# Kernel optimization log

Measured on AMD Instinct MI355X. Metric: run time of the kernel, lower is better.

## Reference

```python
import jax, jax.numpy as jnp
import numpy as np

N_NODES = 32768
N_EDGES = 196608
N_GRAPHS = 256
DEG = 6
HID = 128
RVD = 16
EMB = HID - RVD   # atom/bond embedding dim = hidden - random_vec_dim
VOCAB = 128
TGT = 256
DEPTH = 5
N_AGG = 4         # mean, max, min, std
N_SC = 3          # identity, amplification, attenuation
EPS = 1e-5


def setup_inputs() -> dict:
    key = jax.random.key(0)
    ks = jax.random.split(key, 12)

    def g(i, shape, scale=0.05):
        return jax.random.normal(ks[i], shape, dtype=jnp.float32) * scale

    return {
        "atom_feats": jax.random.randint(ks[0], (N_NODES, 9), 0, 100),
        "bond_feats": jax.random.randint(ks[1], (N_EDGES, 3), 0, 4),
        "src": jax.random.randint(ks[2], (N_EDGES,), 0, N_NODES),
        # every node receives exactly DEG messages (DGL reduce requires in-edges)
        "dst": jnp.repeat(jnp.arange(N_NODES), DEG),
        "graph_ids": jnp.repeat(jnp.arange(N_GRAPHS), N_NODES // N_GRAPHS),
        "n_graphs": N_GRAPHS,
        "rand_x": jax.random.normal(ks[3], (N_NODES, RVD), dtype=jnp.float32),   # std=1.0
        "rand_edge": jax.random.normal(ks[4], (N_EDGES, RVD), dtype=jnp.float32),
        "atom_emb": g(5, (9, VOCAB, EMB)),
        "bond_emb": g(6, (3, VOCAB, EMB)),
        "pre_W": g(7, (DEPTH, 3 * HID, HID)),
        "pre_b": jnp.zeros((DEPTH, HID), jnp.float32),
        "post_W": g(8, (DEPTH, (N_AGG * N_SC + 1) * HID, HID)),
        "post_b": jnp.zeros((DEPTH, HID), jnp.float32),
        "ro_W1": g(9, (3 * HID, HID)),
        "ro_b1": jnp.zeros((HID,), jnp.float32),
        "ro_W2": g(10, (HID, TGT)),
        "ro_b2": jnp.zeros((TGT,), jnp.float32),
    }


def reference(atom_feats, bond_feats, src, dst, graph_ids, n_graphs,
              rand_x, rand_edge, atom_emb, bond_emb,
              pre_W, pre_b, post_W, post_b, ro_W1, ro_b1, ro_W2, ro_b2):
    n = atom_feats.shape[0]
    # OGB-style encoders: sum of per-column embeddings, then concat random vec
    h = jnp.concatenate([atom_emb[jnp.arange(9), atom_feats].sum(1), rand_x], -1)   # [N, HID]
    ef = jnp.concatenate([bond_emb[jnp.arange(3), bond_feats].sum(1), rand_edge], -1)  # [E, HID]

    deg = jax.ops.segment_sum(jnp.ones((dst.shape[0],), h.dtype), dst, n)
    degc = jnp.maximum(deg, 1.0)[:, None]
    logD = jnp.log(deg + 1.0)[:, None]                 # avg_d['log'] = 1.0
    inv_logD = jnp.where(logD > 0, 1.0 / jnp.maximum(logD, EPS), 0.0)

    def layer(hc, p):
        pW, pb, qW, qb = p
        # pretrans MLP on [src_feat, dst_feat, edge_feat]; last_activation = activation (relu)
        z = jnp.concatenate([hc[src], hc[dst], ef], -1)          # [E, 3*HID]
        e = jax.nn.relu(z @ pW + pb)                             # [E, HID]
        s = jax.ops.segment_sum(e, dst, n)
        mean = s / degc
        mean_sq = jax.ops.segment_sum(e * e, dst, n) / degc
        mx = jax.ops.segment_max(e, dst, n)
        mn = jax.ops.segment_min(e, dst, n)
        std = jnp.sqrt(jax.nn.relu(mean_sq - mean * mean) + EPS)
        agg = jnp.concatenate([mean, mx, mn, std], -1)           # [N, 4*HID]
        scaled = jnp.concatenate([agg, agg * logD, agg * inv_logD], -1)  # [N, 12*HID]
        h_new = jnp.concatenate([hc, scaled], -1) @ qW + qb + hc  # posttrans (linear) + residual
        return h_new, None

    h, _ = jax.lax.scan(layer, h, (pre_W, pre_b, post_W, post_b))

    # multi-aggregator readout: mean, sum, max per graph
    cnt = jnp.maximum(jax.ops.segment_sum(jnp.ones((n,), h.dtype), graph_ids, n_graphs), 1.0)[:, None]
    gsum = jax.ops.segment_sum(h, graph_ids, n_graphs)
    gmax = jax.ops.segment_max(h, graph_ids, n_graphs)
    r = jnp.concatenate([gsum / cnt, gsum, gmax], -1)            # [G, 3*HID]
    return jax.nn.relu(r @ ro_W1 + ro_b1) @ ro_W2 + ro_b2        # [G, TGT]
```

## Files before the change

### kernel.cpp

```cpp
#include <hip/hip_runtime.h>
#include <hip/hip_bf16.h>

#define N_NODES 32768
#define N_EDGES 196608
#define N_GRAPHS 256
#define DEG 6
#define HID 128
#define RVD 16
#define EMB 112
#define VOCAB 128
#define TGT 256
#define DEPTH 5

#define LOG7 1.9459101090932196f
#define ILOG7 0.5138983423697507f

typedef __hip_bfloat16 bf16;
using frag_ab = __attribute__((ext_vector_type(8))) short;
using frag_cd = __attribute__((ext_vector_type(4))) float;
typedef float f32x2 __attribute__((ext_vector_type(2)));

static __device__ __forceinline__ float b2f(bf16 x) { return __bfloat162float(x); }
static __device__ __forceinline__ bf16  f2b(float x) { return __float2bfloat16(x); }
static __device__ __forceinline__ float us2f(unsigned short u) {
    unsigned int x = ((unsigned int)u) << 16;
    return __uint_as_float(x);
}
static __device__ __forceinline__ unsigned short f2us(float x) {
    bf16 b = __float2bfloat16(x);
    return *reinterpret_cast<unsigned short*>(&b);
}

#define PB_ENC  16384
#define PB_WB   (PB_ENC + 640)
#define PB_WC   (PB_WB + 1600)
#define PB_WR   (PB_WC + 80)
#define PB_CODE (PB_WR + 768)
#define PB_T    (PB_CODE + 320)

__global__ __launch_bounds__(256) void prep_k(const int* __restrict__ af, const float* __restrict__ rx,
                                              const float* __restrict__ aemb, bf16* __restrict__ h,
                                              const float* __restrict__ preW, const float* __restrict__ preB,
                                              const float* __restrict__ postW,
                                              const int* __restrict__ bfeat, const float* __restrict__ bemb,
                                              bf16* __restrict__ wb, bf16* __restrict__ wc,
                                              bf16* __restrict__ wrB, unsigned char* __restrict__ codeA,
                                              bf16* __restrict__ Tb) {
    int blk = blockIdx.x, tid = threadIdx.x;
    if (blk < PB_ENC) {
        int v = blk * 2 + (tid >> 7), c = tid & 127;
        float val;
        if (c < EMB) {
            val = 0.f;
            #pragma unroll
            for (int i = 0; i < 9; ++i) {
                int f = af[v * 9 + i];
                val += aemb[(i * VOCAB + f) * EMB + c];
            }
        } else {
            val = rx[v * RVD + (c - EMB)];
        }
        h[(size_t)v * HID + c] = f2b(val);
    } else if (blk < PB_WB) {
        int idx = (blk - PB_ENC) * 256 + tid;
        if (idx < DEPTH * 32768) {
            int j = idx & 7, L = (idx >> 3) & 63, nt = (idx >> 9) & 15, ks = (idx >> 13) & 3, l = idx >> 15;
            int k = ks * 32 + ((L >> 4) * 8) + j;
            int n = nt * 16 + (L & 15);
            const float* W = preW + (size_t)l * 384 * 128;
            float v = (n < 128) ? W[k * 128 + n] : W[(128 + k) * 128 + (n - 128)];
            wb[idx] = f2b(v);
        }
    } else if (blk < PB_WC) {
        int idx = (blk - PB_WB) * 256 + tid;
        if (idx < DEPTH * 81920) {
            int j = idx & 7, L = (idx >> 3) & 63, nt = (idx >> 9) & 7;
            int t = idx >> 12;
            int ks = t % 20, l = t / 20;
            int k = ks * 32 + ((L >> 4) * 8) + j;
            int n = nt * 16 + (L & 15);
            const float* W = postW + (size_t)l * 1664 * 128;
            float v;
            if (k < 128) {
                v = W[k * 128 + n];
            } else {
                int jj = k - 128;
                v = W[(128 + jj) * 128 + n] + LOG7 * W[(640 + jj) * 128 + n] + ILOG7 * W[(1152 + jj) * 128 + n];
            }
            wc[idx] = f2b(v);
        }
    } else if (blk < PB_WR) {
        int idx = (blk - PB_WC) * 256 + tid;
        if (idx < DEPTH * 4096) {
            int j = idx & 7, L = (idx >> 3) & 63, nt = (idx >> 9) & 7, l = idx >> 12;
            int k = ((L >> 4) * 8) + j;
            int n = nt * 16 + (L & 15);
            float v = (k < 16) ? preW[(size_t)l * 384 * 128 + (368 + k) * 128 + n] : 0.f;
            wrB[idx] = f2b(v);
        }
    } else if (blk < PB_CODE) {
        int e = (blk - PB_WR) * 256 + tid;
        if (e < N_EDGES)
            codeA[e] = (unsigned char)(bfeat[e * 3] | (bfeat[e * 3 + 1] << 2) | (bfeat[e * 3 + 2] << 4));
    } else {
        if (tid < 128) {
            int t = blk - PB_CODE;
            int l = t >> 6, cd = t & 63, c = tid;
            int f0 = cd & 3, f1 = (cd >> 2) & 3, f2 = cd >> 4;
            const float* W = preW + (size_t)l * 384 * 128 + 256 * 128;
            float acc = preB[l * 128 + c];
            #pragma unroll 4
            for (int k = 0; k < EMB; ++k) {
                float bsk = bemb[(0 * VOCAB + f0) * EMB + k]
                          + bemb[(1 * VOCAB + f1) * EMB + k]
                          + bemb[(2 * VOCAB + f2) * EMB + k];
                acc += bsk * W[k * 128 + c];
            }
            Tb[(size_t)(l * 64 + cd) * 128 + c] = f2b(acc);
        }
    }
}

__global__ __launch_bounds__(256) void gemm_z12(const bf16* __restrict__ A,
                                                const bf16* __restrict__ Bp,
                                                bf16* __restrict__ C) {
    int lane = threadIdx.x & 63;
    int wave = threadIdx.x >> 6;
    int m = lane & 15, quad = lane >> 4;
    int row0 = blockIdx.x * 64 + wave * 16;

    frag_cd acc[16];
    #pragma unroll
    for (int nt = 0; nt < 16; ++nt)
        #pragma unroll
        for (int i = 0; i < 4; ++i) acc[nt][i] = 0.f;

    const frag_ab* Bf = (const frag_ab*)Bp;
    const bf16* arow = A + (size_t)(row0 + m) * 128;
    #pragma unroll
    for (int ks = 0; ks < 4; ++ks) {
        frag_ab a = *(const frag_ab*)(arow + ks * 32 + quad * 8);
        #pragma unroll
        for (int nt = 0; nt < 16; ++nt) {
            frag_ab b = Bf[(ks * 16 + nt) * 64 + lane];
            acc[nt] = __builtin_amdgcn_mfma_f32_16x16x32_bf16(a, b, acc[nt], 0, 0, 0);
        }
    }
    #pragma unroll
    for (int nt = 0; nt < 16; ++nt) {
        int col = nt * 16 + m;
        #pragma unroll
        for (int r = 0; r < 4; ++r) {
            int row = row0 + quad * 4 + r;
            C[(size_t)row * 256 + col] = f2b(acc[nt][r]);
        }
    }
}

__global__ __launch_bounds__(256, 4) void fused_layer(bf16* __restrict__ h,
                                                      const bf16* __restrict__ Zcur,
                                                      const int* __restrict__ src,
                                                      const unsigned char* __restrict__ code,
                                                      const float* __restrict__ rand_edge,
                                                      const bf16* __restrict__ Tb,
                                                      const float* __restrict__ Wr,
                                                      const bf16* __restrict__ Bp,
                                                      const float* __restrict__ bias,
                                                      const bf16* __restrict__ Bn,
                                                      bf16* __restrict__ Znext) {
    __shared__ __align__(16) bf16 agg_lds[32 * 520];
    __shared__ __align__(16) float relds[4][384];

    int tid = threadIdx.x;
    int lane = tid & 63, wave = tid >> 6;
    int ml = lane & 15, quad = lane >> 4;
    int row0 = blockIdx.x * 32;

    const unsigned short* Zu = (const unsigned short*)Zcur;
    const unsigned short* Tu = (const unsigned short*)Tb;
    unsigned short* Ag = (unsigned short*)agg_lds;
    int c = lane * 2;

    {
        const int vbase = row0 + wave * 8;

        f32x2 wr2[16];
        #pragma unroll
        for (int k = 0; k < 16; ++k) {
            float2 w2 = *(const float2*)(Wr + k * 128 + c);
            wr2[k].x = w2.x; wr2[k].y = w2.y;
        }

        {
            const float2* rb = (const float2*)(rand_edge + (size_t)vbase * 96);
            float2 a0 = rb[lane], a1 = rb[lane + 64], a2 = rb[lane + 128];
            float2* rl = (float2*)relds[wave];
            rl[lane] = a0; rl[lane + 64] = a1; rl[lane + 128] = a2;
        }
        float2 rh0, rh1, rh2;

        int svs[2][6]; unsigned short cpk[2][3];
        ushort2 z1u[3][6], tvu[3][6], z2u[3];

#define LOADIDX(node, slot)                                                        \
        {                                                                          \
            const int2* sp = (const int2*)(src + (size_t)(vbase + (node)) * 6);    \
            int2 a_ = sp[0], b_ = sp[1], d_ = sp[2];                               \
            svs[slot][0] = a_.x; svs[slot][1] = a_.y; svs[slot][2] = b_.x;         \
            svs[slot][3] = b_.y; svs[slot][4] = d_.x; svs[slot][5] = d_.y;         \
            const unsigned short* cp = (const unsigned short*)(code + (vbase + (node)) * 6); \
            cpk[slot][0] = cp[0]; cpk[slot][1] = cp[1]; cpk[slot][2] = cp[2];      \
        }

#define GATHER(node, gs, is)                                                       \
        {                                                                          \
            z2u[gs] = *(const ushort2*)(Zu + (size_t)(vbase + (node)) * 256 + 128 + c); \
            _Pragma("unroll")                                                      \
            for (int j = 0; j < 6; ++j)                                            \
                z1u[gs][j] = *(const ushort2*)(Zu + (size_t)svs[is][j] * 256 + c); \
            tvu[gs][0] = *(const ushort2*)(Tu + (cpk[is][0] & 255) * 128 + c);     \
            tvu[gs][1] = *(const ushort2*)(Tu + (cpk[is][0] >> 8) * 128 + c);      \
            tvu[gs][2] = *(const ushort2*)(Tu + (cpk[is][1] & 255) * 128 + c);     \
            tvu[gs][3] = *(const ushort2*)(Tu + (cpk[is][1] >> 8) * 128 + c);      \
            tvu[gs][4] = *(const ushort2*)(Tu + (cpk[is][2] & 255) * 128 + c);     \
            tvu[gs][5] = *(const ushort2*)(Tu + (cpk[is][2] >> 8) * 128 + c);      \
        }

        LOADIDX(0, 0); LOADIDX(1, 1);
        GATHER(0, 0, 0);
        LOADIDX(2, 0);
        GATHER(1, 1, 1);
        LOADIDX(3, 1);

        #pragma unroll
        for (int i = 0; i < 8; ++i) {
            const int s = i % 3;
            if (i == 2) {
                const float2* rb2 = (const float2*)(rand_edge + (size_t)(vbase + 4) * 96);
                rh0 = rb2[lane]; rh1 = rb2[lane + 64]; rh2 = rb2[lane + 128];
            }
            if (i == 4) {
                float2* rl = (float2*)relds[wave];
                rl[lane] = rh0; rl[lane + 64] = rh1; rl[lane + 128] = rh2;
            }
            if (i < 6) GATHER(i + 2, (i + 2) % 3, i & 1);
            if (i < 4) LOADIDX(i + 4, i & 1);

            float z2a = us2f(z2u[s].x), z2b = us2f(z2u[s].y);
            f32x2 s2  = {0.f, 0.f}, ss2 = {0.f, 0.f};
            f32x2 mx2 = {-1e30f, -1e30f}, mn2 = {1e30f, 1e30f};
            #pragma unroll
            for (int j = 0; j < 6; ++j) {
                const float4* rp = (const float4*)&relds[wave][(i & 3) * 96 + j * 16];
                float4 r0 = rp[0], r1 = rp[1], r2 = rp[2], r3 = rp[3];
                f32x2 v2;
                v2.x = us2f(z1u[s][j].x) + z2a + us2f(tvu[s][j].x);
                v2.y = us2f(z1u[s][j].y) + z2b + us2f(tvu[s][j].y);
                float rk[16] = {r0.x, r0.y, r0.z, r0.w, r1.x, r1.y, r1.z, r1.w,
                                r2.x, r2.y, r2.z, r2.w, r3.x, r3.y, r3.z, r3.w};
                #pragma unroll
                for (int k = 0; k < 16; ++k) v2 += rk[k] * wr2[k];
                v2 = __builtin_elementwise_max(v2, (f32x2){0.f, 0.f});
                s2 += v2;
                ss2 += v2 * v2;
                mx2 = __builtin_elementwise_max(mx2, v2);
                mn2 = __builtin_elementwise_min(mn2, v2);
            }
            f32x2 mean2 = s2 * (1.f / 6.f);
            f32x2 msq2  = ss2 * (1.f / 6.f);
            f32x2 var2  = __builtin_elementwise_max(msq2 - mean2 * mean2, (f32x2){0.f, 0.f});
            float sda = sqrtf(var2.x + 1e-5f), sdb = sqrtf(var2.y + 1e-5f);
            int lrow = wave * 8 + i;
            size_t base = (size_t)lrow * 520 + c;
            *(ushort2*)(Ag + base)       = make_ushort2(f2us(mean2.x), f2us(mean2.y));
            *(ushort2*)(Ag + base + 128) = make_ushort2(f2us(mx2.x),   f2us(mx2.y));
            *(ushort2*)(Ag + base + 256) = make_ushort2(f2us(mn2.x),   f2us(mn2.y));
            *(ushort2*)(Ag + base + 384) = make_ushort2(f2us(sda),     f2us(sdb));
        }
#undef LOADIDX
#undef GATHER
    }
    __syncthreads();

    int ng = wave;

    frag_cd acc[2][2];
    #pragma unroll
    for (int m2 = 0; m2 < 2; ++m2)
        #pragma unroll
        for (int nt = 0; nt < 2; ++nt)
            #pragma unroll
            for (int i = 0; i < 4; ++i) acc[m2][nt][i] = 0.f;

    const frag_ab* Bf = (const frag_ab*)Bp;
    #pragma unroll
    for (int ks = 0; ks < 4; ++ks) {
        frag_ab b0 = Bf[(ks * 8 + ng * 2 + 0) * 64 + lane];
        frag_ab b1 = Bf[(ks * 8 + ng * 2 + 1) * 64 + lane];
        #pragma unroll
        for (int m2 = 0; m2 < 2; ++m2) {
            frag_ab a = *(const frag_ab*)(h + (size_t)(row0 + m2 * 16 + ml) * 128 + ks * 32 + quad * 8);
            acc[m2][0] = __builtin_amdgcn_mfma_f32_16x16x32_bf16(a, b0, acc[m2][0], 0, 0, 0);
            acc[m2][1] = __builtin_amdgcn_mfma_f32_16x16x32_bf16(a, b1, acc[m2][1], 0, 0, 0);
        }
    }
    #pragma unroll
    for (int ks = 0; ks < 16; ++ks) {
        frag_ab b0 = Bf[((4 + ks) * 8 + ng * 2 + 0) * 64 + lane];
        frag_ab b1 = Bf[((4 + ks) * 8 + ng * 2 + 1) * 64 + lane];
        #pragma unroll
        for (int m2 = 0; m2 < 2; ++m2) {
            frag_ab a = *(const frag_ab*)(agg_lds + (size_t)(m2 * 16 + ml) * 520 + ks * 32 + quad * 8);
            acc[m2][0] = __builtin_amdgcn_mfma_f32_16x16x32_bf16(a, b0, acc[m2][0], 0, 0, 0);
            acc[m2][1] = __builtin_amdgcn_mfma_f32_16x16x32_bf16(a, b1, acc[m2][1], 0, 0, 0);
        }
    }

    __syncthreads();

    float* pgemm = (float*)agg_lds;
    #pragma unroll
    for (int nt = 0; nt < 2; ++nt) {
        int col = (ng * 2 + nt) * 16 + ml;
        float bs_ = bias[col];
        #pragma unroll
        for (int m2 = 0; m2 < 2; ++m2) {
            #pragma unroll
            for (int r2 = 0; r2 < 4; ++r2) {
                int lr = m2 * 16 + quad * 4 + r2;
                pgemm[lr * 132 + col] = acc[m2][nt][r2] + bs_;
            }
        }
    }
    __syncthreads();

    bf16* newh = agg_lds + 8448;
    {
        int row = tid >> 3, cg = tid & 7;
        const float4* pg = (const float4*)(pgemm + row * 132 + cg * 16);
        float4 p0 = pg[0], p1 = pg[1], p2 = pg[2], p3 = pg[3];
        unsigned short* hrow = (unsigned short*)(h + (size_t)(row0 + row) * 128 + cg * 16);
        frag_ab h0 = *(const frag_ab*)hrow;
        frag_ab h1 = *(const frag_ab*)(hrow + 8);
        float nv[16] = {p0.x, p0.y, p0.z, p0.w, p1.x, p1.y, p1.z, p1.w,
                        p2.x, p2.y, p2.z, p2.w, p3.x, p3.y, p3.z, p3.w};
        #pragma unroll
        for (int j = 0; j < 8; ++j) nv[j]     += us2f((unsigned short)h0[j]);
        #pragma unroll
        for (int j = 0; j < 8; ++j) nv[8 + j] += us2f((unsigned short)h1[j]);
        frag_ab o0, o1;
        #pragma unroll
        for (int j = 0; j < 8; ++j) o0[j] = (short)f2us(nv[j]);
        #pragma unroll
        for (int j = 0; j < 8; ++j) o1[j] = (short)f2us(nv[8 + j]);
        *(frag_ab*)hrow = o0;
        *(frag_ab*)(hrow + 8) = o1;
        *(frag_ab*)&newh[row * 136 + cg * 16] = o0;
        *(frag_ab*)&newh[row * 136 + cg * 16 + 8] = o1;
    }

    if (Bn) {
        __syncthreads();
        const frag_ab* Bf2 = (const frag_ab*)Bn;
        frag_cd a2[2][4];
        #pragma unroll
        for (int m2 = 0; m2 < 2; ++m2)
            #pragma unroll
            for (int nt = 0; nt < 4; ++nt)
                #pragma unroll
                for (int i = 0; i < 4; ++i) a2[m2][nt][i] = 0.f;
        #pragma unroll
        for (int ks = 0; ks < 4; ++ks) {
            frag_ab bb[4];
            #pragma unroll
            for (int nt = 0; nt < 4; ++nt)
                bb[nt] = Bf2[(ks * 16 + ng * 4 + nt) * 64 + lane];
            #pragma unroll
            for (int m2 = 0; m2 < 2; ++m2) {
                frag_ab a = *(const frag_ab*)&newh[(m2 * 16 + ml) * 136 + ks * 32 + quad * 8];
                #pragma unroll
                for (int nt = 0; nt < 4; ++nt)
                    a2[m2][nt] = __builtin_amdgcn_mfma_f32_16x16x32_bf16(a, bb[nt], a2[m2][nt], 0, 0, 0);
            }
        }
        bf16* ztile = agg_lds;
        #pragma unroll
        for (int m2 = 0; m2 < 2; ++m2) {
            #pragma unroll
            for (int nt = 0; nt < 4; ++nt) {
                int col = (ng * 4 + nt) * 16 + ml;
                #pragma unroll
                for (int r2 = 0; r2 < 4; ++r2) {
                    int lr = m2 * 16 + quad * 4 + r2;
                    ztile[lr * 264 + col] = f2b(a2[m2][nt][r2]);
                }
            }
        }
        __syncthreads();
        int row = tid >> 3, cg = tid & 7;
        unsigned short* zr = (unsigned short*)(Znext + (size_t)(row0 + row) * 256 + cg * 32);
        const unsigned short* zs = (const unsigned short*)ztile + row * 264 + cg * 32;
        #pragma unroll
        for (int k2 = 0; k2 < 4; ++k2)
            *(frag_ab*)(zr + k2 * 8) = *(const frag_ab*)(zs + k2 * 8);
    }
}

__global__ __launch_bounds__(128) void readout(const bf16* __restrict__ h, const float* __restrict__ W1,
                                               const float* __restrict__ b1, const float* __restrict__ W2,
                                               const float* __restrict__ b2, float* __restrict__ out) {
    __shared__ float r[384];
    __shared__ float y1[128];
    int g = blockIdx.x, c = threadIdx.x;
    float s = 0.f, mx = -1e30f;
    for (int v = 0; v < 128; ++v) {
        float hv = b2f(h[((size_t)g * 128 + v) * HID + c]);
        s += hv; mx = fmaxf(mx, hv);
    }
    r[c] = s * (1.f / 128.f);
    r[128 + c] = s;
    r[256 + c] = mx;
    __syncthreads();
    float a1 = b1[c];
    for (int k = 0; k < 384; ++k) a1 += r[k] * W1[k * 128 + c];
    y1[c] = fmaxf(a1, 0.f);
    __syncthreads();
    #pragma unroll
    for (int o = 0; o < 2; ++o) {
        int t = c + o * 128;
        float a2 = b2[t];
        for (int k = 0; k < 128; ++k) a2 += y1[k] * W2[k * 256 + t];
        out[(size_t)g * 256 + t] = a2;
    }
}

extern "C" void kernel_launch(void* const* d_in, const int* in_sizes, int n_in,
                              void* d_out, int out_size, void* d_ws, size_t ws_size,
                              hipStream_t stream) {
    const int*   atom_feats = (const int*)d_in[0];
    const int*   bond_feats = (const int*)d_in[1];
    const int*   src        = (const int*)d_in[2];
    const float* rand_x     = (const float*)d_in[6];
    const float* rand_edge  = (const float*)d_in[7];
    const float* atom_emb   = (const float*)d_in[8];
    const float* bond_emb   = (const float*)d_in[9];
    const float* pre_W      = (const float*)d_in[10];
    const float* pre_b      = (const float*)d_in[11];
    const float* post_W     = (const float*)d_in[12];
    const float* post_b     = (const float*)d_in[13];
    const float* ro_W1      = (const float*)d_in[14];
    const float* ro_b1      = (const float*)d_in[15];
    const float* ro_W2      = (const float*)d_in[16];
    const float* ro_b2      = (const float*)d_in[17];

    char* p = (char*)d_ws;
    auto alloc = [&](size_t bytes) {
        char* r = p;
        p += (bytes + 255) & ~(size_t)255;
        return r;
    };
    bf16*  h    = (bf16*) alloc((size_t)N_NODES * HID * 2);
    bf16*  z12a = (bf16*) alloc((size_t)N_NODES * 256 * 2);
    bf16*  z12b = (bf16*) alloc((size_t)N_NODES * 256 * 2);
    bf16*  wb   = (bf16*) alloc((size_t)DEPTH * 32768 * 2);
    bf16*  wc   = (bf16*) alloc((size_t)DEPTH * 81920 * 2);
    bf16*  wrB  = (bf16*) alloc((size_t)DEPTH * 4096 * 2);
    bf16*  Tb   = (bf16*) alloc((size_t)DEPTH * 64 * 128 * 2);
    unsigned char* code = (unsigned char*)alloc(N_EDGES);

    prep_k<<<PB_T, 256, 0, stream>>>(atom_feats, rand_x, atom_emb, h,
                                     pre_W, pre_b, post_W,
                                     bond_feats, bond_emb,
                                     wb, wc, wrB, code, Tb);

    gemm_z12<<<N_NODES / 64, 256, 0, stream>>>(h, wb, z12a);

    bf16* zc = z12a;
    bf16* zn = z12b;
    for (int l = 0; l < DEPTH; ++l) {
        const bf16* wbn = (l + 1 < DEPTH) ? (wb + (size_t)(l + 1) * 32768) : nullptr;
        fused_layer<<<N_NODES / 32, 256, 0, stream>>>(
            h, zc, src, code, rand_edge,
            Tb + (size_t)l * 8192,
            pre_W + (size_t)l * 384 * 128 + 368 * 128,
            wc + (size_t)l * 81920,
            post_b + l * HID,
            wbn, zn);
        bf16* t = zc; zc = zn; zn = t;
    }

    readout<<<N_GRAPHS, 128, 0, stream>>>(h, ro_W1, ro_b1, ro_W2, ro_b2, (float*)d_out);
}
```

Before: 336.7 us.

## Compute random-edge projection with MFMA into LDS instead of scalar FMAs

Replaces the per-lane 16-term scalar FMA projection of rand_edge through the last 16 rows of pre_W with a bf16 MFMA over two nodes (12 edges) at a time. The results go to a per-wave bf16 LDS buffer that the aggregation loop reads back. This removes the register-heavy float weight array and the LDS float staging, and the launch-bounds occupancy hint is lowered from 4 to 3. In exchange the projection is now rounded to bf16, half the MFMA rows are padding, and each wave writes to LDS and reads it back without an explicit barrier.

```diff
diff --git a/kernel.cpp b/kernel.cpp
--- a/kernel.cpp
+++ b/kernel.cpp
@@ -22,6 +22,10 @@
 
 static __device__ __forceinline__ float b2f(bf16 x) { return __bfloat162float(x); }
 static __device__ __forceinline__ bf16  f2b(float x) { return __float2bfloat16(x); }
+static __device__ __forceinline__ short f2s(float x) {
+    bf16 b = __float2bfloat16(x);
+    return *reinterpret_cast<short*>(&b);
+}
 static __device__ __forceinline__ float us2f(unsigned short u) {
     unsigned int x = ((unsigned int)u) << 16;
     return __uint_as_float(x);
@@ -157,19 +161,19 @@
     }
 }
 
-__global__ __launch_bounds__(256, 4) void fused_layer(bf16* __restrict__ h,
+__global__ __launch_bounds__(256, 3) void fused_layer(bf16* __restrict__ h,
                                                       const bf16* __restrict__ Zcur,
                                                       const int* __restrict__ src,
                                                       const unsigned char* __restrict__ code,
                                                       const float* __restrict__ rand_edge,
                                                       const bf16* __restrict__ Tb,
-                                                      const float* __restrict__ Wr,
+                                                      const bf16* __restrict__ WrB,
                                                       const bf16* __restrict__ Bp,
                                                       const float* __restrict__ bias,
                                                       const bf16* __restrict__ Bn,
                                                       bf16* __restrict__ Znext) {
     __shared__ __align__(16) bf16 agg_lds[32 * 520];
-    __shared__ __align__(16) float relds[4][384];
+    __shared__ __align__(16) bf16 rdot_lds[4][16 * 136];
 
     int tid = threadIdx.x;
     int lane = tid & 63, wave = tid >> 6;
@@ -183,24 +187,14 @@
 
     {
         const int vbase = row0 + wave * 8;
-
-        f32x2 wr2[16];
-        #pragma unroll
-        for (int k = 0; k < 16; ++k) {
-            float2 w2 = *(const float2*)(Wr + k * 128 + c);
-            wr2[k].x = w2.x; wr2[k].y = w2.y;
-        }
-
-        {
-            const float2* rb = (const float2*)(rand_edge + (size_t)vbase * 96);
-            float2 a0 = rb[lane], a1 = rb[lane + 64], a2 = rb[lane + 128];
-            float2* rl = (float2*)relds[wave];
-            rl[lane] = a0; rl[lane + 64] = a1; rl[lane + 128] = a2;
-        }
-        float2 rh0, rh1, rh2;
-
-        int svs[2][6]; unsigned short cpk[2][3];
+        bf16* rdw = &rdot_lds[wave][0];
+        const unsigned short* rdu = (const unsigned short*)rdw;
+        const frag_ab* BfR = (const frag_ab*)WrB;
+        const int me = (ml < 12) ? ml : 11;
+
+        int svs[2][6]; int cds[2][6];
         ushort2 z1u[3][6], tvu[3][6], z2u[3];
+        float4 reA, reB;
 
 #define LOADIDX(node, slot)                                                        \
         {                                                                          \
@@ -209,7 +203,9 @@
             svs[slot][0] = a_.x; svs[slot][1] = a_.y; svs[slot][2] = b_.x;         \
             svs[slot][3] = b_.y; svs[slot][4] = d_.x; svs[slot][5] = d_.y;         \
             const unsigned short* cp = (const unsigned short*)(code + (vbase + (node)) * 6); \
-            cpk[slot][0] = cp[0]; cpk[slot][1] = cp[1]; cpk[slot][2] = cp[2];      \
+            unsigned short x_ = cp[0], y_ = cp[1], z_ = cp[2];                     \
+            cds[slot][0] = x_ & 255; cds[slot][1] = x_ >> 8; cds[slot][2] = y_ & 255; \
+            cds[slot][3] = y_ >> 8;  cds[slot][4] = z_ & 255; cds[slot][5] = z_ >> 8; \
         }
 
 #define GATHER(node, gs, is)                                                       \
@@ -218,14 +214,15 @@
             _Pragma("unroll")                                                      \
             for (int j = 0; j < 6; ++j)                                            \
                 z1u[gs][j] = *(const ushort2*)(Zu + (size_t)svs[is][j] * 256 + c); \
-            tvu[gs][0] = *(const ushort2*)(Tu + (cpk[is][0] & 255) * 128 + c);     \
-            tvu[gs][1] = *(const ushort2*)(Tu + (cpk[is][0] >> 8) * 128 + c);      \
-            tvu[gs][2] = *(const ushort2*)(Tu + (cpk[is][1] & 255) * 128 + c);     \
-            tvu[gs][3] = *(const ushort2*)(Tu + (cpk[is][1] >> 8) * 128 + c);      \
-            tvu[gs][4] = *(const ushort2*)(Tu + (cpk[is][2] & 255) * 128 + c);     \
-            tvu[gs][5] = *(const ushort2*)(Tu + (cpk[is][2] >> 8) * 128 + c);      \
-        }
-
+            _Pragma("unroll")                                                      \
+            for (int j = 0; j < 6; ++j)                                            \
+                tvu[gs][j] = *(const ushort2*)(Tu + cds[is][j] * 128 + c);         \
+        }
+
+        if (quad < 2) {
+            const float4* rp = (const float4*)(rand_edge + (size_t)(vbase * 6 + me) * 16 + quad * 8);
+            reA = rp[0]; reB = rp[1];
+        }
         LOADIDX(0, 0); LOADIDX(1, 1);
         GATHER(0, 0, 0);
         LOADIDX(2, 0);
@@ -235,31 +232,50 @@
         #pragma unroll
         for (int i = 0; i < 8; ++i) {
             const int s = i % 3;
-            if (i == 2) {
-                const float2* rb2 = (const float2*)(rand_edge + (size_t)(vbase + 4) * 96);
-                rh0 = rb2[lane]; rh1 = rb2[lane + 64]; rh2 = rb2[lane + 128];
-            }
-            if (i == 4) {
-                float2* rl = (float2*)relds[wave];
-                rl[lane] = rh0; rl[lane + 64] = rh1; rl[lane + 128] = rh2;
-            }
+
+            if ((i & 1) == 0) {
+                frag_ab a;
+                if (quad < 2) {
+                    a[0] = f2s(reA.x); a[1] = f2s(reA.y); a[2] = f2s(reA.z); a[3] = f2s(reA.w);
+                    a[4] = f2s(reB.x); a[5] = f2s(reB.y); a[6] = f2s(reB.z); a[7] = f2s(reB.w);
+                } else {
+                    #pragma unroll
+                    for (int j = 0; j < 8; ++j) a[j] = 0;
+                }
+                #pragma unroll
+                for (int nt = 0; nt < 8; ++nt) {
+                    frag_cd acc4;
+                    #pragma unroll
+                    for (int q = 0; q < 4; ++q) acc4[q] = 0.f;
+                    acc4 = __builtin_amdgcn_mfma_f32_16x16x32_bf16(a, BfR[nt * 64 + lane], acc4, 0, 0, 0);
+                    #pragma unroll
+                    for (int r = 0; r < 4; ++r)
+                        rdw[(quad * 4 + r) * 136 + nt * 16 + ml] = f2b(acc4[r]);
+                }
+                if (i < 6 && quad < 2) {
+                    const float4* rp = (const float4*)(rand_edge
+                        + (size_t)((vbase + i + 2) * 6 + me) * 16 + quad * 8);
+                    reA = rp[0]; reB = rp[1];
+                }
+            }
+
             if (i < 6) GATHER(i + 2, (i + 2) % 3, i & 1);
             if (i < 4) LOADIDX(i + 4, i & 1);
 
+            ushort2 rdv[6];
+            {
+                const unsigned short* rb = rdu + ((i & 1) * 6) * 136 + c;
+                #pragma unroll
+                for (int j = 0; j < 6; ++j) rdv[j] = *(const ushort2*)(rb + j * 136);
+            }
             float z2a = us2f(z2u[s].x), z2b = us2f(z2u[s].y);
             f32x2 s2  = {0.f, 0.f}, ss2 = {0.f, 0.f};
             f32x2 mx2 = {-1e30f, -1e30f}, mn2 = {1e30f, 1e30f};
             #pragma unroll
             for (int j = 0; j < 6; ++j) {
-                const float4* rp = (const float4*)&relds[wave][(i & 3) * 96 + j * 16];
-                float4 r0 = rp[0], r1 = rp[1], r2 = rp[2], r3 = rp[3];
                 f32x2 v2;
-                v2.x = us2f(z1u[s][j].x) + z2a + us2f(tvu[s][j].x);
-                v2.y = us2f(z1u[s][j].y) + z2b + us2f(tvu[s][j].y);
-                float rk[16] = {r0.x, r0.y, r0.z, r0.w, r1.x, r1.y, r1.z, r1.w,
-                                r2.x, r2.y, r2.z, r2.w, r3.x, r3.y, r3.z, r3.w};
-                #pragma unroll
-                for (int k = 0; k < 16; ++k) v2 += rk[k] * wr2[k];
+                v2.x = us2f(z1u[s][j].x) + z2a + us2f(tvu[s][j].x) + us2f(rdv[j].x);
+                v2.y = us2f(z1u[s][j].y) + z2b + us2f(tvu[s][j].y) + us2f(rdv[j].y);
                 v2 = __builtin_elementwise_max(v2, (f32x2){0.f, 0.f});
                 s2 += v2;
                 ss2 += v2 * v2;
@@ -482,7 +498,7 @@
         fused_layer<<<N_NODES / 32, 256, 0, stream>>>(
             h, zc, src, code, rand_edge,
             Tb + (size_t)l * 8192,
-            pre_W + (size_t)l * 384 * 128 + 368 * 128,
+            wrB + (size_t)l * 4096,
             wc + (size_t)l * 81920,
             post_b + l * HID,
             wbn, zn);
```

After: 326.5 us. 3.0% less time.
